# Optimization experiments

Hardware: AMD Instinct MI355X
Metric: run time of the kernel (lower is better)

## Reference

```python
import jax, jax.numpy as jnp
import numpy as np
from jax import lax

B, N, C, T = 8, 2000, 32, 12
K, F_CHEV, F_TIME = 3, 64, 64
LN_EPS = 1e-5


def setup_inputs() -> dict:
    key = jax.random.key(0)
    ks = jax.random.split(key, 20)
    s = 0.1
    return {
        "x": jax.random.normal(ks[0], (B, N, C, T), jnp.float32),
        "cheb_polys": jax.random.normal(ks[1], (K, N, N), jnp.float32) * 0.02,
        # temporal attention params
        "U1": jax.random.normal(ks[2], (N,), jnp.float32) * s,
        "U2": jax.random.normal(ks[3], (C, N), jnp.float32) * s,
        "U3": jax.random.normal(ks[4], (C,), jnp.float32) * s,
        "be": jax.random.normal(ks[5], (1, T, T), jnp.float32) * s,
        "Ve": jax.random.normal(ks[6], (T, T), jnp.float32) * s,
        # spatial attention params
        "W1": jax.random.normal(ks[7], (T,), jnp.float32) * s,
        "W2": jax.random.normal(ks[8], (C, T), jnp.float32) * s,
        "W3": jax.random.normal(ks[9], (C,), jnp.float32) * s,
        "bs": jax.random.normal(ks[10], (1, N, N), jnp.float32) * s,
        "Vs": jax.random.normal(ks[11], (N, N), jnp.float32) * (s / np.sqrt(N)),
        # Chebyshev conv params, stacked (K, C, F_chev)
        "Theta": jax.random.normal(ks[12], (K, C, F_CHEV), jnp.float32) * (1.0 / np.sqrt(C)),
        # time conv (1x3) and residual conv (1x1), NCHW/OIHW layout
        "tc_w": jax.random.normal(ks[13], (F_TIME, F_CHEV, 1, 3), jnp.float32) * (1.0 / np.sqrt(3 * F_CHEV)),
        "tc_b": jnp.zeros((F_TIME,), jnp.float32),
        "rc_w": jax.random.normal(ks[14], (F_TIME, C, 1, 1), jnp.float32) * (1.0 / np.sqrt(C)),
        "rc_b": jnp.zeros((F_TIME,), jnp.float32),
        # LayerNorm over nb_time_filter
        "ln_g": jnp.ones((F_TIME,), jnp.float32),
        "ln_b": jnp.zeros((F_TIME,), jnp.float32),
    }


def _conv2d(x, w, b, stride_t):
    # x: (B, Cin, N, T), w: (Cout, Cin, kh, kw)
    pad_w = (w.shape[3] - 1) // 2
    y = lax.conv_general_dilated(
        x, w, window_strides=(1, stride_t),
        padding=[(0, 0), (pad_w, pad_w)],
        dimension_numbers=("NCHW", "OIHW", "NCHW"))
    return y + b[None, :, None, None]


def reference(x, cheb_polys, U1, U2, U3, be, Ve, W1, W2, W3, bs, Vs,
              Theta, tc_w, tc_b, rc_w, rc_b, ln_g, ln_b):
    b, n, c, t = x.shape

    # ---- temporal attention: (B, T, T) ----
    lhs = jnp.einsum("bnct,n->btc", x, U1)              # x.permute(0,3,2,1) @ U1
    lhs = jnp.einsum("btc,cn->btn", lhs, U2)
    rhs = jnp.einsum("c,bnct->bnt", U3, x)
    E = jnp.einsum("ij,bjk->bik", Ve,
                   jax.nn.sigmoid(jnp.einsum("btn,bnu->btu", lhs, rhs) + be))
    temporal_At = jax.nn.softmax(E, axis=1)             # (B, T, T)

    # apply temporal attention
    x_TAt = jnp.matmul(x.reshape(b, n * c, t), temporal_At).reshape(b, n, c, t)

    # ---- spatial attention on x_TAt: (B, N, N) ----
    lhs_s = jnp.einsum("bnct,t->bnc", x_TAt, W1)
    lhs_s = jnp.einsum("bnc,ct->bnt", lhs_s, W2)
    rhs_s = jnp.einsum("c,bnct->btn", W3, x_TAt)        # (W3 @ x).transpose(-1,-2)
    S = jnp.einsum("ij,bjk->bik", Vs,
                   jax.nn.sigmoid(jnp.einsum("bnt,btm->bnm", lhs_s, rhs_s) + bs))
    spatial_At = jax.nn.softmax(S, axis=1)              # (B, N, N)

    # ---- Chebyshev graph conv with spatial attention ----
    # A[b,k,j,i] = cheb[k,j,i] * SAt[b,j,i]; out = relu(sum_k A^T x Theta_k)
    A = cheb_polys[None, :, :, :] * spatial_At[:, None, :, :]   # (B, K, N, N)
    h = jnp.einsum("bkji,bjct->bkitc", A, x)                    # (B, K, N, T, C)
    spatial_gcn = jax.nn.relu(jnp.einsum("bkitc,kcf->bift", h, Theta))  # (B, N, F, T)

    # ---- temporal conv + residual + LayerNorm ----
    time_out = _conv2d(spatial_gcn.transpose(0, 2, 1, 3), tc_w, tc_b, 1)  # (B, F_time, N, T')
    x_res = _conv2d(x.transpose(0, 2, 1, 3), rc_w, rc_b, 1)               # (B, F_time, N, T')
    z = jax.nn.relu(x_res + time_out).transpose(0, 3, 2, 1)               # (B, T', N, F_time)

    mu = jnp.mean(z, axis=-1, keepdims=True)
    var = jnp.mean((z - mu) ** 2, axis=-1, keepdims=True)
    zn = (z - mu) * lax.rsqrt(var + LN_EPS) * ln_g + ln_b

    return zn.transpose(0, 2, 3, 1)                                       # (B, N, F_time, T')
```

## Files before the change

kernel.cpp:

```cpp
#include <hip/hip_runtime.h>
#include <hip/hip_bf16.h>
#include <math.h>

#define B_ 8
#define N_ 2000
#define C_ 32
#define T_ 12
#define K_ 3
#define FC_ 64
#define FT_ 64
#define PW 2048

typedef short bf16x8 __attribute__((ext_vector_type(8)));
typedef float f32x4 __attribute__((ext_vector_type(4)));

__device__ __forceinline__ float sigmoidf(float v) { return 1.0f / (1.0f + __expf(-v)); }
__device__ __forceinline__ float bf2f(unsigned short u) {
    union { unsigned int i; float f; } v; v.i = ((unsigned int)u) << 16; return v.f;
}
__device__ __forceinline__ unsigned short f2bf(float f) {
    union { __hip_bfloat16 h; unsigned short u; } v; v.h = __float2bfloat16(f); return v.u;
}
typedef const __attribute__((address_space(1))) void* gas_t;
typedef __attribute__((address_space(3))) void* las_t;
__device__ __forceinline__ void gload16(const unsigned short* g, unsigned short* l) {
    __builtin_amdgcn_global_load_lds((gas_t)g, (las_t)l, 16, 0, 0);
}

__global__ __launch_bounds__(256) void k_tprep(const float* __restrict__ x, const float* __restrict__ U1,
                                               const float* __restrict__ U3,
                                               float* __restrict__ rhsT, float* __restrict__ plh) {
    int b = blockIdx.y, chunk = blockIdx.x;
    int tid = threadIdx.x;
    int nl = tid >> 5, c = tid & 31;
    int w = tid >> 6;
    float u3 = U3[c];
    float plA[12];
#pragma unroll
    for (int t = 0; t < 12; ++t) plA[t] = 0.f;
    for (int it = 0; it < 5; ++it) {
        int n = chunk * 40 + it * 8 + nl;
        const float* xp = x + ((size_t)(b * 2000 + n) * 32 + c) * 12;
        float4 v0 = *(const float4*)xp, v1 = *(const float4*)(xp + 4), v2 = *(const float4*)(xp + 8);
        float xv[12] = {v0.x, v0.y, v0.z, v0.w, v1.x, v1.y, v1.z, v1.w, v2.x, v2.y, v2.z, v2.w};
        float rv[12];
#pragma unroll
        for (int t = 0; t < 12; ++t) rv[t] = u3 * xv[t];
#pragma unroll
        for (int off = 16; off >= 1; off >>= 1)
#pragma unroll
            for (int t = 0; t < 12; ++t) rv[t] += __shfl_xor(rv[t], off);
        if (c == 0) {
#pragma unroll
            for (int t = 0; t < 12; ++t) rhsT[(size_t)(b * 2000 + n) * 12 + t] = rv[t];
        }
        float u1 = U1[n];
#pragma unroll
        for (int t = 0; t < 12; ++t) plA[t] += u1 * xv[t];
    }
#pragma unroll
    for (int t = 0; t < 12; ++t) plA[t] += __shfl_xor(plA[t], 32);
    __shared__ float accs[4][32][12];
    if ((tid & 63) < 32) {
#pragma unroll
        for (int t = 0; t < 12; ++t) accs[w][c][t] = plA[t];
    }
    __syncthreads();
    if (tid < 384) {
        int c2 = tid / 12, t2 = tid % 12;
        float s = accs[0][c2][t2] + accs[1][c2][t2] + accs[2][c2][t2] + accs[3][c2][t2];
        plh[((size_t)(b * 50 + chunk)) * 384 + tid] = s;
    }
}

__global__ __launch_bounds__(256) void k_tred(const float* __restrict__ plh, float* __restrict__ lhs1) {
    int b = blockIdx.x;
    for (int q = threadIdx.x; q < 384; q += 256) {
        const float* p = plh + (size_t)b * 50 * 384 + q;
        float s = 0.f;
        for (int ch = 0; ch < 50; ++ch) s += p[(size_t)ch * 384];
        int c = q / 12, t = q % 12;
        lhs1[(b * 12 + t) * 32 + c] = s;
    }
}

__global__ __launch_bounds__(256) void k_lhsT(const float* __restrict__ lhs1, const float* __restrict__ U2,
                                              float* __restrict__ lhsT) {
    int gid = blockIdx.x * 256 + threadIdx.x;
    if (gid >= B_ * T_ * N_) return;
    int n = gid % N_;
    int bt = gid / N_;
    const float* l1 = lhs1 + bt * C_;
    float a = 0.f;
#pragma unroll
    for (int c = 0; c < C_; ++c) a += l1[c] * U2[c * N_ + n];
    lhsT[gid] = a;
}

__global__ __launch_bounds__(256) void k_tatt1(const float* __restrict__ lhsT, const float* __restrict__ rhsT,
                                               float* __restrict__ pP) {
    int b = blockIdx.y, ch = blockIdx.x;
    int tid = threadIdx.x;
    int n0 = ch * 125;
    __shared__ float sL[12][128];
    __shared__ float sR[128][12];
    for (int q = tid; q < 12 * 125; q += 256) {
        int t = q / 125, nn = q % 125;
        sL[t][nn] = lhsT[(size_t)(b * 12 + t) * 2000 + n0 + nn];
    }
    for (int q = tid; q < 125 * 12; q += 256) {
        int nn = q / 12, t = q % 12;
        sR[nn][t] = rhsT[(size_t)(b * 2000 + n0 + nn) * 12 + t];
    }
    __syncthreads();
    if (tid < 144) {
        int tP = tid / 12, uP = tid % 12;
        float a = 0.f;
#pragma unroll 5
        for (int nn = 0; nn < 125; ++nn) a += sL[tP][nn] * sR[nn][uP];
        pP[(size_t)(b * 16 + ch) * 144 + tid] = a;
    }
}

__global__ __launch_bounds__(256) void k_tatt2(const float* __restrict__ pP, const float* __restrict__ be,
                                               const float* __restrict__ Ve, float* __restrict__ At) {
    int b = blockIdx.x, tid = threadIdx.x;
    __shared__ float sp[144], sE[144], mk[12], sk[12];
    int tP = tid / 12, uP = tid % 12;
    if (tid < 144) {
        float a = 0.f;
#pragma unroll
        for (int ch = 0; ch < 16; ++ch) a += pP[(size_t)(b * 16 + ch) * 144 + tid];
        sp[tid] = sigmoidf(a + be[tid]);
    }
    __syncthreads();
    if (tid < 144) {
        float e = 0.f;
#pragma unroll
        for (int j = 0; j < 12; ++j) e += Ve[tP * 12 + j] * sp[j * 12 + uP];
        sE[tid] = e;
    }
    __syncthreads();
    if (tid < 12) {
        float m = -1e30f;
#pragma unroll
        for (int i = 0; i < 12; ++i) m = fmaxf(m, sE[i * 12 + tid]);
        float s = 0.f;
#pragma unroll
        for (int i = 0; i < 12; ++i) s += __expf(sE[i * 12 + tid] - m);
        mk[tid] = m; sk[tid] = 1.0f / s;
    }
    __syncthreads();
    if (tid < 144) At[b * 144 + tid] = __expf(sE[tid] - mk[uP]) * sk[uP];
}

__global__ __launch_bounds__(256) void k_xsp(const float* __restrict__ x, const float* __restrict__ At,
                                             const float* __restrict__ W1, const float* __restrict__ W2,
                                             const float* __restrict__ W3,
                                             float* __restrict__ lhs_s, float* __restrict__ rhs_s) {
    int b = blockIdx.y, chunk = blockIdx.x;
    int tid = threadIdx.x, nl = tid >> 5, c = tid & 31;
    int n = chunk * 8 + nl;
    __shared__ float atl[144];
    __shared__ float w2l[384];
    __shared__ float w1l[12];
    if (tid < 144) atl[tid] = At[b * 144 + tid];
    if (tid >= 144 && tid < 156) w1l[tid - 144] = W1[tid - 144];
    for (int q = tid; q < 384; q += 256) w2l[q] = W2[q];
    __syncthreads();
    const float* xp = x + ((size_t)(b * 2000 + n) * 32 + c) * 12;
    float4 v0 = *(const float4*)xp, v1 = *(const float4*)(xp + 4), v2 = *(const float4*)(xp + 8);
    float xv[12] = {v0.x, v0.y, v0.z, v0.w, v1.x, v1.y, v1.z, v1.w, v2.x, v2.y, v2.z, v2.w};
    float xa[12];
#pragma unroll
    for (int t = 0; t < 12; ++t) {
        float s = 0.f;
#pragma unroll
        for (int u = 0; u < 12; ++u) s += xv[u] * atl[u * 12 + t];
        xa[t] = s;
    }
    float w3 = W3[c];
    float rv[12], lv[12];
    float l1 = 0.f;
#pragma unroll
    for (int t = 0; t < 12; ++t) l1 += xa[t] * w1l[t];
#pragma unroll
    for (int t = 0; t < 12; ++t) { rv[t] = w3 * xa[t]; lv[t] = l1 * w2l[c * 12 + t]; }
#pragma unroll
    for (int off = 16; off >= 1; off >>= 1)
#pragma unroll
        for (int t = 0; t < 12; ++t) { rv[t] += __shfl_xor(rv[t], off); lv[t] += __shfl_xor(lv[t], off); }
    if (c == 0) {
#pragma unroll
        for (int t = 0; t < 12; ++t) rhs_s[(size_t)(b * 12 + t) * 2000 + n] = rv[t];
#pragma unroll
        for (int t = 0; t < 12; ++t) lhs_s[(size_t)(b * 2000 + n) * 12 + t] = lv[t];
    }
}

__global__ __launch_bounds__(256) void k_wprep(const float* __restrict__ tc_w, const float* __restrict__ rc_w,
                                               float* __restrict__ tcwT, float* __restrict__ rcwT) {
    int gid = blockIdx.x * 256 + threadIdx.x;
    if (gid < 12288) {
        int fi = gid / 192, rem = gid % 192, f = rem / 3, d = rem % 3;
        tcwT[gid] = tc_w[(f * 64 + fi) * 3 + d];
    } else if (gid < 14336) {
        int q = gid - 12288;
        int c = q >> 6, f = q & 63;
        rcwT[q] = rc_w[f * 32 + c];
    }
}

__global__ __launch_bounds__(256) void k_vsb(const float* __restrict__ Vs, unsigned short* __restrict__ Vsb) {
    int gid = blockIdx.x * 256 + threadIdx.x;
    int row = gid >> 8, chunk = gid & 255;
    int p0 = chunk * 8;
    unsigned short o[8];
#pragma unroll
    for (int e = 0; e < 8; ++e) {
        int p = p0 + e;
        o[e] = (row < N_ && p < N_) ? f2bf(Vs[row * N_ + p]) : (unsigned short)0;
    }
    *(int4*)(Vsb + (size_t)row * PW + p0) = *(int4*)o;
}

__global__ __launch_bounds__(256) void k_chebT(const float* __restrict__ cheb, unsigned short* __restrict__ chebT) {
    int j0 = blockIdx.x * 64, i0 = blockIdx.y * 64, kk = blockIdx.z;
    __shared__ float Tl[64][65];
    int t = threadIdx.x;
    int rr = t >> 2, c0 = (t & 3) * 16;
    int j = j0 + rr;
#pragma unroll
    for (int e = 0; e < 16; ++e) {
        int i = i0 + c0 + e;
        Tl[rr][c0 + e] = (j < N_ && i < N_) ? cheb[(size_t)kk * 4000000 + (size_t)j * N_ + i] : 0.f;
    }
    __syncthreads();
    int l = t & 63, w = t >> 6;
    unsigned short o[16];
#pragma unroll
    for (int e = 0; e < 16; ++e) o[e] = f2bf(Tl[w * 16 + e][l]);
    unsigned short* dst = chebT + (size_t)kk * PW * PW + (size_t)(i0 + l) * PW + j0 + w * 16;
    *(int4*)dst = *(int4*)o;
    *(int4*)(dst + 8) = *(int4*)(o + 8);
}

__global__ __launch_bounds__(256) void k_xT(const float* __restrict__ x, unsigned short* __restrict__ xT) {
    int j0 = blockIdx.x * 64, r0 = blockIdx.y * 64, b = blockIdx.z;
    __shared__ float Tl[64][65];
    int t = threadIdx.x;
    int rr = t >> 2, c0 = (t & 3) * 16;
    int j = j0 + rr;
#pragma unroll
    for (int e = 0; e < 16; ++e) {
        int r = r0 + c0 + e;
        Tl[rr][c0 + e] = (j < N_) ? x[(size_t)(b * N_ + j) * 384 + r] : 0.f;
    }
    __syncthreads();
    int l = t & 63, w = t >> 6;
    unsigned short o[16];
#pragma unroll
    for (int e = 0; e < 16; ++e) o[e] = f2bf(Tl[w * 16 + e][l]);
    unsigned short* dst = xT + (size_t)b * 384 * PW + (size_t)(r0 + l) * PW + j0 + w * 16;
    *(int4*)dst = *(int4*)o;
    *(int4*)(dst + 8) = *(int4*)(o + 8);
}

__global__ __launch_bounds__(256) void k_sig(const float* __restrict__ lhs_s, const float* __restrict__ rhs_s,
                                             const float* __restrict__ bs, unsigned short* __restrict__ sigT) {
    int p0 = blockIdx.x * 64, i0 = blockIdx.y * 64, b = blockIdx.z;
    __shared__ float sL[64][12];
    __shared__ float sR[12][64];
    __shared__ float bsl[64][65];
    int t = threadIdx.x;
    for (int q = t; q < 768; q += 256) {
        int pp = q / 12, tt = q % 12;
        int p = p0 + pp;
        sL[pp][tt] = (p < N_) ? lhs_s[(b * N_ + p) * 12 + tt] : 0.f;
    }
    for (int q = t; q < 768; q += 256) {
        int tt = q >> 6, ii = q & 63;
        int i = i0 + ii;
        sR[tt][ii] = (i < N_) ? rhs_s[b * (T_ * N_) + tt * N_ + i] : 0.f;
    }
    {
        int pp = t >> 2, c0 = (t & 3) * 16;
        int p = p0 + pp;
        if (p < N_ && i0 + c0 + 15 < N_) {
            const float* src = bs + (size_t)p * N_ + i0 + c0;
#pragma unroll
            for (int e = 0; e < 16; e += 4) *(float4*)&bsl[pp][c0 + e] = *(const float4*)(src + e);
        } else {
#pragma unroll
            for (int e = 0; e < 16; ++e) {
                int i = i0 + c0 + e;
                bsl[pp][c0 + e] = (p < N_ && i < N_) ? bs[(size_t)p * N_ + i] : 0.f;
            }
        }
    }
    __syncthreads();
    int ii = t & 63, w = t >> 6;
    int i = i0 + ii;
    unsigned short o[16];
#pragma unroll
    for (int e = 0; e < 16; ++e) {
        int pl = w * 16 + e;
        int p = p0 + pl;
        float v = 0.f;
        if (p < N_ && i < N_) {
            float d = bsl[pl][ii];
#pragma unroll
            for (int tt = 0; tt < 12; ++tt) d += sL[pl][tt] * sR[tt][ii];
            v = sigmoidf(d);
        }
        o[e] = f2bf(v);
    }
    unsigned short* dst = sigT + (size_t)b * PW * PW + (size_t)i * PW + p0 + w * 16;
    *(int4*)dst = *(int4*)o;
    *(int4*)(dst + 8) = *(int4*)(o + 8);
}

#define FR_(R) (((R) ^ ((R) >> 2)) & 3)
__global__ __launch_bounds__(512) void k_gemm_S_mfma(const unsigned short* __restrict__ Vsb,
                                                     const unsigned short* __restrict__ sigT,
                                                     unsigned short* __restrict__ ST) {
    int lid = blockIdx.x + (blockIdx.y << 3) + (blockIdx.z << 6);
    int swz = (lid & 7) * 64 + (lid >> 3);
    int j0 = (swz & 7) * 256;
    int i0 = ((swz >> 3) & 7) * 256;
    int b = swz >> 6;
    const unsigned short* Ap = sigT + (size_t)b * PW * PW;
    __shared__ unsigned short As[2][2][8192];
    __shared__ unsigned short Bs[2][2][8192];
    int t = threadIdx.x, lane = t & 63, w = t >> 6;
    int wr = w >> 2, wc = w & 3;
    int l15 = lane & 15, kseg = lane >> 4;
    f32x4 acc[8][4];
#pragma unroll
    for (int m = 0; m < 8; ++m)
#pragma unroll
        for (int n = 0; n < 4; ++n)
#pragma unroll
            for (int q = 0; q < 4; ++q) acc[m][n][q] = 0.f;
    int srow = t >> 2;
    int gchunk = ((t & 3) ^ FR_(srow)) * 8;
    const unsigned short* gA = Ap + (size_t)(i0 + srow) * PW + gchunk;
    const unsigned short* gB = Vsb + (size_t)(j0 + srow) * PW + gchunk;
    int ldw = w * 512;
#define SA_(buf_, kt_, kh_) do { \
    gload16(gA + (size_t)(kt_) * 64 + (kh_) * 32, &As[buf_][kh_][ldw]); \
    gload16(gA + (size_t)128 * PW + (size_t)(kt_) * 64 + (kh_) * 32, &As[buf_][kh_][4096 + ldw]); \
} while (0)
#define SB_(buf_, kt_, kh_) do { \
    gload16(gB + (size_t)(kt_) * 64 + (kh_) * 32, &Bs[buf_][kh_][ldw]); \
    gload16(gB + (size_t)128 * PW + (size_t)(kt_) * 64 + (kh_) * 32, &Bs[buf_][kh_][4096 + ldw]); \
} while (0)
#define RDA(kh_, buf_) { _Pragma("unroll") for (int m = 0; m < 8; ++m) { \
    int R = wr * 128 + m * 16 + l15; \
    aR[m] = *(const bf16x8*)&As[buf_][kh_][R * 32 + ((kseg ^ FR_(R)) << 3)]; } }
#define RDB(kh_, nh_, buf_) { _Pragma("unroll") for (int n = 0; n < 2; ++n) { \
    int R = wc * 64 + (nh_) * 32 + n * 16 + l15; \
    bR[n] = *(const bf16x8*)&Bs[buf_][kh_][R * 32 + ((kseg ^ FR_(R)) << 3)]; } }
#define LGKM0 do { asm volatile("s_waitcnt lgkmcnt(0)" ::: "memory"); __builtin_amdgcn_sched_barrier(0); } while (0)
#define MMA(nh_) do { __builtin_amdgcn_s_setprio(1); \
    _Pragma("unroll") for (int m = 0; m < 8; ++m) \
    _Pragma("unroll") for (int n = 0; n < 2; ++n) \
        acc[m][(nh_) * 2 + n] = __builtin_amdgcn_mfma_f32_16x16x32_bf16(aR[m], bR[n], acc[m][(nh_) * 2 + n], 0, 0, 0); \
    __builtin_amdgcn_s_setprio(0); } while (0)
    SA_(0, 0, 0); SB_(0, 0, 0); SA_(0, 0, 1); SB_(0, 0, 1);
    SA_(1, 1, 0); SB_(1, 1, 0);
    asm volatile("s_waitcnt vmcnt(4)" ::: "memory");
    __builtin_amdgcn_s_barrier();
    for (int kt = 0; kt < 32; ++kt) {
        int cur = kt & 1, nb = cur ^ 1;
        bf16x8 aR[8], bR[2];
        RDA(0, cur); RDB(0, 0, cur);
        if (kt + 1 < 32) SA_(nb, kt + 1, 1);
        __builtin_amdgcn_s_barrier();
        LGKM0;
        MMA(0);
        __builtin_amdgcn_s_barrier();
        RDB(0, 1, cur);
        if (kt + 1 < 32) SB_(nb, kt + 1, 1);
        __builtin_amdgcn_s_barrier();
        LGKM0;
        MMA(1);
        __builtin_amdgcn_s_barrier();
        RDA(1, cur); RDB(1, 0, cur);
        if (kt + 2 < 32) SA_(cur, kt + 2, 0);
        __builtin_amdgcn_s_barrier();
        LGKM0;
        MMA(0);
        __builtin_amdgcn_s_barrier();
        RDB(1, 1, cur);
        if (kt + 2 < 32) SB_(cur, kt + 2, 0);
        __builtin_amdgcn_s_barrier();
        LGKM0;
        MMA(1);
        if (kt < 30) asm volatile("s_waitcnt vmcnt(4)" ::: "memory");
        else         asm volatile("s_waitcnt vmcnt(0)" ::: "memory");
        __builtin_amdgcn_s_barrier();
    }
#undef SA_
#undef SB_
#undef RDA
#undef RDB
#undef LGKM0
#undef MMA
    unsigned short* Sp = ST + (size_t)b * PW * PW;
#pragma unroll
    for (int m = 0; m < 8; ++m) {
        int row0 = i0 + wr * 128 + m * 16 + (kseg << 2);
#pragma unroll
        for (int n = 0; n < 4; ++n) {
            int col = j0 + wc * 64 + (n >> 1) * 32 + (n & 1) * 16 + l15;
#pragma unroll
            for (int q = 0; q < 4; ++q)
                Sp[(size_t)(row0 + q) * PW + col] = f2bf(acc[m][n][q]);
        }
    }
}

__global__ __launch_bounds__(256) void k_smrow(const unsigned short* __restrict__ ST,
                                               float* __restrict__ gm, float* __restrict__ gs) {
    int wid = threadIdx.x >> 6, lane = threadIdx.x & 63;
    int b = blockIdx.y;
    int i = blockIdx.x * 4 + wid;
    const unsigned short* rp = ST + (size_t)b * PW * PW + (size_t)i * PW;
    float vals[32];
    float m = -1e30f;
#pragma unroll
    for (int k = 0; k < 4; ++k) {
        int j0 = lane * 8 + k * 512;
        if (j0 < N_) {
            union { int4 v; unsigned short s[8]; } u;
            u.v = *(const int4*)(rp + j0);
#pragma unroll
            for (int e = 0; e < 8; ++e) {
                vals[k * 8 + e] = bf2f(u.s[e]);
                m = fmaxf(m, vals[k * 8 + e]);
            }
        } else {
#pragma unroll
            for (int e = 0; e < 8; ++e) vals[k * 8 + e] = -1e30f;
        }
    }
#pragma unroll
    for (int off = 32; off >= 1; off >>= 1) m = fmaxf(m, __shfl_xor(m, off));
    float s = 0.f;
#pragma unroll
    for (int k = 0; k < 32; ++k) s += __expf(vals[k] - m);
#pragma unroll
    for (int off = 32; off >= 1; off >>= 1) s += __shfl_xor(s, off);
    if (lane == 0) {
        gm[b * 2048 + i] = m;
        gs[b * 2048 + i] = 1.0f / s;
    }
}

__global__ __launch_bounds__(512) void k_gemm_cheb_mfma(const unsigned short* __restrict__ chebT,
                                                        const unsigned short* __restrict__ ST,
                                                        const float* __restrict__ gm, const float* __restrict__ gs,
                                                        const unsigned short* __restrict__ xT,
                                                        unsigned short* __restrict__ h2) {
    int bk = blockIdx.y;
    int b = bk / 3, kk = bk % 3;
    int i0 = blockIdx.x * 128;
    const unsigned short* Ac = chebT + (size_t)kk * PW * PW;
    const unsigned short* Sa = ST + (size_t)b * PW * PW;
    const unsigned short* Bx = xT + (size_t)b * 384 * PW;
    __shared__ unsigned short As[2][4096];
    __shared__ unsigned short Bs[2][12288];
    int t = threadIdx.x, lane = t & 63, w = t >> 6;
    int wr = w >> 2, wc = w & 3;
    f32x4 acc[4][6];
#pragma unroll
    for (int a = 0; a < 4; ++a)
#pragma unroll
        for (int c = 0; c < 6; ++c)
#pragma unroll
            for (int q = 0; q < 4; ++q) acc[a][c][q] = 0.f;
    int arow = t >> 2, aq = t & 3;
    const unsigned short* gc = Ac + (size_t)(i0 + arow) * PW + aq * 8;
    const unsigned short* gsat = Sa + (size_t)(i0 + arow) * PW + aq * 8;
    float gmv = gm[b * 2048 + i0 + arow];
    float gsv = gs[b * 2048 + i0 + arow];
    int aoff = arow * 32 + (aq ^ (arow & 3)) * 8;
    int bseg = (t & 3) ^ ((t >> 2) & 3);
    const unsigned short* gB = Bx + (size_t)(t >> 2) * PW + bseg * 8;
    int ldso = w * 512;
#define STAGE_B(buf, p) do { \
    gload16(gB + (p), &Bs[buf][ldso]); \
    gload16(gB + 128 * PW + (p), &Bs[buf][4096 + ldso]); \
    gload16(gB + 256 * PW + (p), &Bs[buf][8192 + ldso]); \
} while (0)
    union U8 { int4 v; unsigned short s[8]; };
    U8 ca, sa;
    ca.v = *(const int4*)gc;
    sa.v = *(const int4*)gsat;
    STAGE_B(0, 0);
    {
        U8 o;
#pragma unroll
        for (int e = 0; e < 8; ++e) o.s[e] = f2bf(bf2f(ca.s[e]) * __expf(bf2f(sa.s[e]) - gmv) * gsv);
        *(int4*)&As[0][aoff] = o.v;
    }
    ca.v = *(const int4*)(gc + 32);
    sa.v = *(const int4*)(gsat + 32);
    __syncthreads();
    int cur = 0;
    int rswz = ((lane >> 4) ^ (lane & 3)) * 8;
    for (int p = 0; p < PW; p += 32) {
        if (p + 32 < PW) {
            STAGE_B(cur ^ 1, p + 32);
            U8 o;
#pragma unroll
            for (int e = 0; e < 8; ++e) o.s[e] = f2bf(bf2f(ca.s[e]) * __expf(bf2f(sa.s[e]) - gmv) * gsv);
            *(int4*)&As[cur ^ 1][aoff] = o.v;
            int pn = (p + 64 < PW) ? p + 64 : 0;
            ca.v = *(const int4*)(gc + pn);
            sa.v = *(const int4*)(gsat + pn);
        }
        bf16x8 af[4], bfr[6];
#pragma unroll
        for (int fm = 0; fm < 4; ++fm)
            af[fm] = *(const bf16x8*)&As[cur][(wr * 64 + fm * 16 + (lane & 15)) * 32 + rswz];
#pragma unroll
        for (int fn = 0; fn < 6; ++fn)
            bfr[fn] = *(const bf16x8*)&Bs[cur][(wc * 96 + fn * 16 + (lane & 15)) * 32 + rswz];
#pragma unroll
        for (int fm = 0; fm < 4; ++fm)
#pragma unroll
            for (int fn = 0; fn < 6; ++fn)
                acc[fm][fn] = __builtin_amdgcn_mfma_f32_16x16x32_bf16(af[fm], bfr[fn], acc[fm][fn], 0, 0, 0);
        __syncthreads();
        cur ^= 1;
    }
#undef STAGE_B
    unsigned short* hp = h2 + (size_t)bk * 768000;
#pragma unroll
    for (int fm = 0; fm < 4; ++fm) {
        int row0 = i0 + wr * 64 + fm * 16 + ((lane >> 4) << 2);
#pragma unroll
        for (int fn = 0; fn < 6; ++fn) {
            int col = wc * 96 + fn * 16 + (lane & 15);
#pragma unroll
            for (int q = 0; q < 4; ++q) {
                int row = row0 + q;
                if (row < N_) hp[(size_t)row * 384 + col] = f2bf(acc[fm][fn][q]);
            }
        }
    }
}

__global__ __launch_bounds__(512) void k_final3(const float* __restrict__ x, const unsigned short* __restrict__ h2,
                                                const float* __restrict__ ThetaG,
                                                const float* __restrict__ tcwT, const float* __restrict__ tc_b,
                                                const float* __restrict__ rcwT, const float* __restrict__ rc_b,
                                                const float* __restrict__ ln_g, const float* __restrict__ ln_b,
                                                float* __restrict__ out) {
    __shared__ __align__(16) char smem[110848];
    unsigned int* gl = (unsigned int*)smem;
    unsigned short* th = (unsigned short*)(smem + 98560);
    float* red_s = (float*)(smem + 98560);
    float* red_q = red_s + 64 * 13;

    int tid = threadIdx.x;
    int n_l = tid & 63, fg = tid >> 6;
    int b = blockIdx.y;
    int node = blockIdx.x * 64 + n_l;
    bool ok = node < N_;
    int nd = ok ? node : N_ - 1;

    for (int q = tid; q < 6144; q += 512) th[q] = f2bf(ThetaG[q]);
    __syncthreads();

    float acc[8][12];
#pragma unroll
    for (int ff = 0; ff < 8; ++ff)
#pragma unroll
        for (int t = 0; t < 12; ++t) acc[ff][t] = 0.f;
    const unsigned short* hb = h2 + (size_t)b * 3 * 768000 + (size_t)nd * 384;
#pragma unroll
    for (int kk = 0; kk < 3; ++kk) {
        const unsigned short* hp = hb + (size_t)kk * 768000;
#pragma unroll 2
        for (int c = 0; c < 32; ++c) {
            const unsigned short* hq = hp + c * 12;
            uint2 u0 = *(const uint2*)(hq);
            uint2 u1 = *(const uint2*)(hq + 4);
            uint2 u2 = *(const uint2*)(hq + 8);
            float h[12];
            h[0] = bf2f((unsigned short)u0.x);  h[1] = bf2f((unsigned short)(u0.x >> 16));
            h[2] = bf2f((unsigned short)u0.y);  h[3] = bf2f((unsigned short)(u0.y >> 16));
            h[4] = bf2f((unsigned short)u1.x);  h[5] = bf2f((unsigned short)(u1.x >> 16));
            h[6] = bf2f((unsigned short)u1.y);  h[7] = bf2f((unsigned short)(u1.y >> 16));
            h[8] = bf2f((unsigned short)u2.x);  h[9] = bf2f((unsigned short)(u2.x >> 16));
            h[10] = bf2f((unsigned short)u2.y); h[11] = bf2f((unsigned short)(u2.y >> 16));
            const unsigned short* wv = th + (kk * 32 + c) * 64 + fg * 8;
            uint2 w01 = *(const uint2*)wv;
            uint2 w23 = *(const uint2*)(wv + 4);
            float wf[8];
            wf[0] = bf2f((unsigned short)w01.x); wf[1] = bf2f((unsigned short)(w01.x >> 16));
            wf[2] = bf2f((unsigned short)w01.y); wf[3] = bf2f((unsigned short)(w01.y >> 16));
            wf[4] = bf2f((unsigned short)w23.x); wf[5] = bf2f((unsigned short)(w23.x >> 16));
            wf[6] = bf2f((unsigned short)w23.y); wf[7] = bf2f((unsigned short)(w23.y >> 16));
#pragma unroll
            for (int ff = 0; ff < 8; ++ff)
#pragma unroll
                for (int t = 0; t < 12; ++t) acc[ff][t] = fmaf(h[t], wf[ff], acc[ff][t]);
        }
    }
    unsigned int* gr = gl + n_l * 385 + fg * 48;
#pragma unroll
    for (int ff = 0; ff < 8; ++ff)
#pragma unroll
        for (int tp = 0; tp < 6; ++tp) {
            float a0 = fmaxf(acc[ff][2 * tp], 0.f), a1 = fmaxf(acc[ff][2 * tp + 1], 0.f);
            gr[ff * 6 + tp] = (unsigned int)f2bf(a0) | ((unsigned int)f2bf(a1) << 16);
        }
    __syncthreads();

    float z[8][12];
#pragma unroll
    for (int ff = 0; ff < 8; ++ff) {
        float bias = tc_b[fg * 8 + ff] + rc_b[fg * 8 + ff];
#pragma unroll
        for (int t = 0; t < 12; ++t) z[ff][t] = bias;
    }
    const float* xp = x + (size_t)(b * 2000 + nd) * 384;
#pragma unroll 2
    for (int c = 0; c < 32; ++c) {
        float4 x0 = *(const float4*)(xp + c * 12);
        float4 x1 = *(const float4*)(xp + c * 12 + 4);
        float4 x2 = *(const float4*)(xp + c * 12 + 8);
        float xv[12] = {x0.x, x0.y, x0.z, x0.w, x1.x, x1.y, x1.z, x1.w, x2.x, x2.y, x2.z, x2.w};
        float4 r0 = *(const float4*)(rcwT + c * 64 + fg * 8);
        float4 r1 = *(const float4*)(rcwT + c * 64 + fg * 8 + 4);
        float rw[8] = {r0.x, r0.y, r0.z, r0.w, r1.x, r1.y, r1.z, r1.w};
#pragma unroll
        for (int ff = 0; ff < 8; ++ff)
#pragma unroll
            for (int t = 0; t < 12; ++t) z[ff][t] = fmaf(xv[t], rw[ff], z[ff][t]);
    }
    const unsigned int* grow = gl + n_l * 385;
    for (int fi = 0; fi < 64; ++fi) {
        float g[12];
#pragma unroll
        for (int j = 0; j < 6; ++j) {
            unsigned int u = grow[fi * 6 + j];
            g[2 * j] = bf2f((unsigned short)u);
            g[2 * j + 1] = bf2f((unsigned short)(u >> 16));
        }
        const float* wp = tcwT + (fi * 64 + fg * 8) * 3;
        float4 w0 = *(const float4*)(wp);
        float4 w1 = *(const float4*)(wp + 4);
        float4 w2 = *(const float4*)(wp + 8);
        float4 w3 = *(const float4*)(wp + 12);
        float4 w4 = *(const float4*)(wp + 16);
        float4 w5 = *(const float4*)(wp + 20);
        float wb[24] = {w0.x, w0.y, w0.z, w0.w, w1.x, w1.y, w1.z, w1.w,
                        w2.x, w2.y, w2.z, w2.w, w3.x, w3.y, w3.z, w3.w,
                        w4.x, w4.y, w4.z, w4.w, w5.x, w5.y, w5.z, w5.w};
#pragma unroll
        for (int ff = 0; ff < 8; ++ff) {
            float a0 = wb[ff * 3], a1 = wb[ff * 3 + 1], a2 = wb[ff * 3 + 2];
            z[ff][0] = fmaf(g[0], a1, fmaf(g[1], a2, z[ff][0]));
#pragma unroll
            for (int t = 1; t < 11; ++t)
                z[ff][t] = fmaf(g[t - 1], a0, fmaf(g[t], a1, fmaf(g[t + 1], a2, z[ff][t])));
            z[ff][11] = fmaf(g[10], a0, fmaf(g[11], a1, z[ff][11]));
        }
    }
#pragma unroll
    for (int ff = 0; ff < 8; ++ff)
#pragma unroll
        for (int t = 0; t < 12; ++t) z[ff][t] = fmaxf(z[ff][t], 0.f);

    float s[12], q[12];
#pragma unroll
    for (int t = 0; t < 12; ++t) { s[t] = 0.f; q[t] = 0.f; }
#pragma unroll
    for (int ff = 0; ff < 8; ++ff)
#pragma unroll
        for (int t = 0; t < 12; ++t) { s[t] += z[ff][t]; q[t] += z[ff][t] * z[ff][t]; }
    __syncthreads();
    for (int g = 0; g < 8; ++g) {
        if (fg == g) {
            if (g == 0) {
#pragma unroll
                for (int t = 0; t < 12; ++t) { red_s[n_l * 13 + t] = s[t]; red_q[n_l * 13 + t] = q[t]; }
            } else {
#pragma unroll
                for (int t = 0; t < 12; ++t) { red_s[n_l * 13 + t] += s[t]; red_q[n_l * 13 + t] += q[t]; }
            }
        }
        __syncthreads();
    }
    float mu[12], rs[12];
#pragma unroll
    for (int t = 0; t < 12; ++t) {
        float m = red_s[n_l * 13 + t] * (1.0f / 64.0f);
        float v = red_q[n_l * 13 + t] * (1.0f / 64.0f) - m * m;
        mu[t] = m;
        rs[t] = rsqrtf(v + 1e-5f);
    }
    if (ok) {
        float* op = out + ((size_t)(b * 2000 + node) * 64 + fg * 8) * 12;
#pragma unroll
        for (int ff = 0; ff < 8; ++ff) {
            float lg = ln_g[fg * 8 + ff], lb = ln_b[fg * 8 + ff];
            float o[12];
#pragma unroll
            for (int t = 0; t < 12; ++t) o[t] = (z[ff][t] - mu[t]) * rs[t] * lg + lb;
#pragma unroll
            for (int tq = 0; tq < 3; ++tq)
                *(float4*)(op + ff * 12 + tq * 4) = make_float4(o[tq * 4], o[tq * 4 + 1], o[tq * 4 + 2], o[tq * 4 + 3]);
        }
    }
}

extern "C" void kernel_launch(void* const* d_in, const int* in_sizes, int n_in,
                              void* d_out, int out_size, void* d_ws, size_t ws_size,
                              hipStream_t stream) {
    const float* x     = (const float*)d_in[0];
    const float* cheb  = (const float*)d_in[1];
    const float* U1    = (const float*)d_in[2];
    const float* U2    = (const float*)d_in[3];
    const float* U3    = (const float*)d_in[4];
    const float* be    = (const float*)d_in[5];
    const float* Ve    = (const float*)d_in[6];
    const float* W1    = (const float*)d_in[7];
    const float* W2    = (const float*)d_in[8];
    const float* W3    = (const float*)d_in[9];
    const float* bs    = (const float*)d_in[10];
    const float* Vs    = (const float*)d_in[11];
    const float* Theta = (const float*)d_in[12];
    const float* tc_w  = (const float*)d_in[13];
    const float* tc_b  = (const float*)d_in[14];
    const float* rc_w  = (const float*)d_in[15];
    const float* rc_b  = (const float*)d_in[16];
    const float* ln_g  = (const float*)d_in[17];
    const float* ln_b  = (const float*)d_in[18];
    float* out = (float*)d_out;

    float* ws    = (float*)d_ws;
    float* At    = ws;
    float* lhs1  = ws + 1152;
    float* lhsT  = ws + 4224;
    float* rhsT  = ws + 196224;
    float* lhs_s = ws + 388224;
    float* rhs_s = ws + 580224;
    float* gm    = ws + 772224;
    float* gs    = ws + 788608;
    float* tcwT  = ws + 804992;
    float* rcwT  = ws + 817280;
    float* plh   = ws + 819328;
    float* pP    = ws + 972928;
    unsigned short* Vsb   = (unsigned short*)(ws + 991360);
    unsigned short* chebT = (unsigned short*)(ws + 3088512);
    unsigned short* xT    = (unsigned short*)(ws + 9379968);
    unsigned short* sigT  = (unsigned short*)(ws + 12525696);
    unsigned short* h2    = sigT;
    unsigned short* STb   = (unsigned short*)(ws + 29302912);

    k_wprep<<<56, 256, 0, stream>>>(tc_w, rc_w, tcwT, rcwT);
    k_vsb<<<2048, 256, 0, stream>>>(Vs, Vsb);
    k_chebT<<<dim3(32, 32, 3), 256, 0, stream>>>(cheb, chebT);
    k_xT<<<dim3(32, 6, 8), 256, 0, stream>>>(x, xT);
    k_tprep<<<dim3(50, 8), 256, 0, stream>>>(x, U1, U3, rhsT, plh);
    k_tred<<<8, 256, 0, stream>>>(plh, lhs1);
    k_lhsT<<<750, 256, 0, stream>>>(lhs1, U2, lhsT);
    k_tatt1<<<dim3(16, 8), 256, 0, stream>>>(lhsT, rhsT, pP);
    k_tatt2<<<8, 256, 0, stream>>>(pP, be, Ve, At);
    k_xsp<<<dim3(250, 8), 256, 0, stream>>>(x, At, W1, W2, W3, lhs_s, rhs_s);
    k_sig<<<dim3(32, 32, 8), 256, 0, stream>>>(lhs_s, rhs_s, bs, sigT);
    k_gemm_S_mfma<<<dim3(8, 8, 8), 512, 0, stream>>>(Vsb, sigT, STb);
    k_smrow<<<dim3(512, 8), 256, 0, stream>>>(STb, gm, gs);
    k_gemm_cheb_mfma<<<dim3(16, 24), 512, 0, stream>>>(chebT, STb, gm, gs, xT, h2);
    k_final3<<<dim3(32, 8), 512, 0, stream>>>(x, h2, Theta, tcwT, tc_b, rcwT, rc_b, ln_g, ln_b, out);
}
```

Measured before the change: 603.6 us.

## Restructure Chebyshev MFMA GEMM into a barrier-phased K-half pipeline with prefetch

Rewrites the main loop of the Chebyshev GEMM kernel to use K tiles of 64, each split into two 32-wide halves, with double-buffered LDS per half. Global prefetch now runs two tiles ahead. Each tile is processed in four barrier-separated phases that interleave LDS fragment reads, the on-the-fly softmax-scaled A tile writes, direct-to-LDS B loads and MFMA bursts, with s_setprio raised around the MFMAs. The goal is to hide global and LDS latency behind matrix math and to halve the number of outer loop iterations. The cost is more barriers, double the LDS footprint, and reliance on explicit waitcnt placement for correctness of the async B loads.

```diff
diff --git a/kernel.cpp b/kernel.cpp
--- a/kernel.cpp
+++ b/kernel.cpp
@@ -469,10 +469,11 @@
     const unsigned short* Ac = chebT + (size_t)kk * PW * PW;
     const unsigned short* Sa = ST + (size_t)b * PW * PW;
     const unsigned short* Bx = xT + (size_t)b * 384 * PW;
-    __shared__ unsigned short As[2][4096];
-    __shared__ unsigned short Bs[2][12288];
+    __shared__ unsigned short As[2][2][4096];
+    __shared__ unsigned short Bs[2][2][12288];
     int t = threadIdx.x, lane = t & 63, w = t >> 6;
     int wr = w >> 2, wc = w & 3;
+    int l15 = lane & 15, kseg = lane >> 4;
     f32x4 acc[4][6];
 #pragma unroll
     for (int a = 0; a < 4; ++a)
@@ -480,70 +481,81 @@
         for (int c = 0; c < 6; ++c)
 #pragma unroll
             for (int q = 0; q < 4; ++q) acc[a][c][q] = 0.f;
-    int arow = t >> 2, aq = t & 3;
-    const unsigned short* gc = Ac + (size_t)(i0 + arow) * PW + aq * 8;
-    const unsigned short* gsat = Sa + (size_t)(i0 + arow) * PW + aq * 8;
+    int arow = t >> 2, achk = t & 3;
+    const unsigned short* gac = Ac + (size_t)(i0 + arow) * PW + achk * 8;
+    const unsigned short* gsa = Sa + (size_t)(i0 + arow) * PW + achk * 8;
     float gmv = gm[b * 2048 + i0 + arow];
     float gsv = gs[b * 2048 + i0 + arow];
-    int aoff = arow * 32 + (aq ^ (arow & 3)) * 8;
-    int bseg = (t & 3) ^ ((t >> 2) & 3);
-    const unsigned short* gB = Bx + (size_t)(t >> 2) * PW + bseg * 8;
-    int ldso = w * 512;
-#define STAGE_B(buf, p) do { \
-    gload16(gB + (p), &Bs[buf][ldso]); \
-    gload16(gB + 128 * PW + (p), &Bs[buf][4096 + ldso]); \
-    gload16(gB + 256 * PW + (p), &Bs[buf][8192 + ldso]); \
+    int awoff = arow * 32 + ((achk ^ FR_(arow)) << 3);
+    int brow = t >> 2;
+    int bchk = ((t & 3) ^ FR_(brow)) * 8;
+    const unsigned short* gB = Bx + (size_t)brow * PW + bchk;
+    int ldw = w * 512;
+    union U8 { int4 v; unsigned short s[8]; };
+#define SB_(buf_, kt_, kh_) do { \
+    gload16(gB + (size_t)(kt_) * 64 + (kh_) * 32, &Bs[buf_][kh_][ldw]); \
+    gload16(gB + (size_t)128 * PW + (size_t)(kt_) * 64 + (kh_) * 32, &Bs[buf_][kh_][4096 + ldw]); \
+    gload16(gB + (size_t)256 * PW + (size_t)(kt_) * 64 + (kh_) * 32, &Bs[buf_][kh_][8192 + ldw]); \
 } while (0)
-    union U8 { int4 v; unsigned short s[8]; };
-    U8 ca, sa;
-    ca.v = *(const int4*)gc;
-    sa.v = *(const int4*)gsat;
-    STAGE_B(0, 0);
+#define WRA(buf_, kh_, cc, ss) do { U8 o_; \
+    _Pragma("unroll") for (int e = 0; e < 8; ++e) \
+        o_.s[e] = f2bf(bf2f((cc).s[e]) * __expf(bf2f((ss).s[e]) - gmv) * gsv); \
+    *(int4*)&As[buf_][kh_][awoff] = o_.v; } while (0)
+#define RDA(kh_, buf_) { _Pragma("unroll") for (int m = 0; m < 4; ++m) { \
+    int R = wr * 64 + m * 16 + l15; \
+    aR[m] = *(const bf16x8*)&As[buf_][kh_][R * 32 + ((kseg ^ FR_(R)) << 3)]; } }
+#define RDB(kh_, nh_, buf_) { _Pragma("unroll") for (int n = 0; n < 3; ++n) { \
+    int R = wc * 96 + (nh_) * 48 + n * 16 + l15; \
+    bR[n] = *(const bf16x8*)&Bs[buf_][kh_][R * 32 + ((kseg ^ FR_(R)) << 3)]; } }
+#define LGKM0 do { asm volatile("s_waitcnt lgkmcnt(0)" ::: "memory"); __builtin_amdgcn_sched_barrier(0); } while (0)
+#define BAR __builtin_amdgcn_s_barrier()
+#define MMA(nh_) do { __builtin_amdgcn_s_setprio(1); \
+    _Pragma("unroll") for (int m = 0; m < 4; ++m) \
+    _Pragma("unroll") for (int n = 0; n < 3; ++n) \
+        acc[m][(nh_) * 3 + n] = __builtin_amdgcn_mfma_f32_16x16x32_bf16(aR[m], bR[n], acc[m][(nh_) * 3 + n], 0, 0, 0); \
+    __builtin_amdgcn_s_setprio(0); } while (0)
     {
-        U8 o;
-#pragma unroll
-        for (int e = 0; e < 8; ++e) o.s[e] = f2bf(bf2f(ca.s[e]) * __expf(bf2f(sa.s[e]) - gmv) * gsv);
-        *(int4*)&As[0][aoff] = o.v;
-    }
-    ca.v = *(const int4*)(gc + 32);
-    sa.v = *(const int4*)(gsat + 32);
-    __syncthreads();
-    int cur = 0;
-    int rswz = ((lane >> 4) ^ (lane & 3)) * 8;
-    for (int p = 0; p < PW; p += 32) {
-        if (p + 32 < PW) {
-            STAGE_B(cur ^ 1, p + 32);
-            U8 o;
-#pragma unroll
-            for (int e = 0; e < 8; ++e) o.s[e] = f2bf(bf2f(ca.s[e]) * __expf(bf2f(sa.s[e]) - gmv) * gsv);
-            *(int4*)&As[cur ^ 1][aoff] = o.v;
-            int pn = (p + 64 < PW) ? p + 64 : 0;
-            ca.v = *(const int4*)(gc + pn);
-            sa.v = *(const int4*)(gsat + pn);
-        }
-        bf16x8 af[4], bfr[6];
-#pragma unroll
-        for (int fm = 0; fm < 4; ++fm)
-            af[fm] = *(const bf16x8*)&As[cur][(wr * 64 + fm * 16 + (lane & 15)) * 32 + rswz];
-#pragma unroll
-        for (int fn = 0; fn < 6; ++fn)
-            bfr[fn] = *(const bf16x8*)&Bs[cur][(wc * 96 + fn * 16 + (lane & 15)) * 32 + rswz];
-#pragma unroll
-        for (int fm = 0; fm < 4; ++fm)
-#pragma unroll
-            for (int fn = 0; fn < 6; ++fn)
-                acc[fm][fn] = __builtin_amdgcn_mfma_f32_16x16x32_bf16(af[fm], bfr[fn], acc[fm][fn], 0, 0, 0);
-        __syncthreads();
-        cur ^= 1;
-    }
-#undef STAGE_B
+        U8 cc, ss;
+        cc.v = *(const int4*)(gac);      ss.v = *(const int4*)(gsa);      WRA(0, 0, cc, ss);
+        cc.v = *(const int4*)(gac + 32); ss.v = *(const int4*)(gsa + 32); WRA(0, 1, cc, ss);
+        cc.v = *(const int4*)(gac + 64); ss.v = *(const int4*)(gsa + 64); WRA(1, 0, cc, ss);
+        cc.v = *(const int4*)(gac + 96); ss.v = *(const int4*)(gsa + 96); WRA(1, 1, cc, ss);
+    }
+    SB_(0, 0, 0); SB_(0, 0, 1); SB_(1, 1, 0); SB_(1, 1, 1);
+    asm volatile("s_waitcnt vmcnt(0) lgkmcnt(0)" ::: "memory");
+    BAR;
+    for (int kt = 0; kt < 32; ++kt) {
+        int cur = kt & 1;
+        bf16x8 aR[4], bR[3];
+        U8 ca0, sa0, ca1, sa1;
+        bool pf = (kt + 2 < 32);
+        RDA(0, cur); RDB(0, 0, cur);
+        if (pf) { ca0.v = *(const int4*)(gac + (size_t)(kt + 2) * 64); sa0.v = *(const int4*)(gsa + (size_t)(kt + 2) * 64); }
+        BAR; LGKM0; MMA(0); BAR;
+        RDB(0, 1, cur);
+        if (pf) { ca1.v = *(const int4*)(gac + (size_t)(kt + 2) * 64 + 32); sa1.v = *(const int4*)(gsa + (size_t)(kt + 2) * 64 + 32); }
+        BAR; LGKM0; MMA(1); BAR;
+        RDA(1, cur); RDB(1, 0, cur);
+        if (pf) { WRA(cur, 0, ca0, sa0); SB_(cur, kt + 2, 0); }
+        BAR; LGKM0; MMA(0); BAR;
+        RDB(1, 1, cur);
+        if (pf) { WRA(cur, 1, ca1, sa1); SB_(cur, kt + 2, 1); }
+        BAR; LGKM0; MMA(1); BAR;
+    }
+#undef SB_
+#undef WRA
+#undef RDA
+#undef RDB
+#undef LGKM0
+#undef BAR
+#undef MMA
     unsigned short* hp = h2 + (size_t)bk * 768000;
 #pragma unroll
     for (int fm = 0; fm < 4; ++fm) {
-        int row0 = i0 + wr * 64 + fm * 16 + ((lane >> 4) << 2);
+        int row0 = i0 + wr * 64 + fm * 16 + (kseg << 2);
 #pragma unroll
         for (int fn = 0; fn < 6; ++fn) {
-            int col = wc * 96 + fn * 16 + (lane & 15);
+            int col = wc * 96 + fn * 16 + l15;
 #pragma unroll
             for (int q = 0; q < 4; ++q) {
                 int row = row0 + q;
```

Result: no change. 602.3 us (-0.2%).
